# Performance work log

Hardware: AMD Instinct MI355X
Metric: run time of the kernel (lower is better)

## Reference

```python
import jax, jax.numpy as jnp
import numpy as np
from jax import lax

C = 16  # channels

def _conv1x1(x, w, b):
    # 1x1x1 Conv3d == channel-mixing einsum. x: [B,C,T,H,W], w: [O,C], b: [O]
    return jnp.einsum('oc,bcthw->bothw', w, x) + b[None, :, None, None, None]

def _ffn(x, w1, b1, w2, b2):
    return _conv1x1(jnp.tanh(_conv1x1(x, w1, b1)), w2, b2)

def setup_inputs() -> dict:
    key = jax.random.key(0)
    ks = jax.random.split(key, 12)
    s = 0.1
    x = jax.random.normal(ks[0], (2, C, 31, 256, 256), dtype=jnp.float32)
    mk_w = lambda k: jax.random.normal(k, (C, C), dtype=jnp.float32) * s
    mk_b = lambda k: jax.random.normal(k, (C,), dtype=jnp.float32) * s
    return {
        'x': x,
        'wf1': mk_w(ks[1]), 'bf1': mk_b(ks[2]),
        'wf2': mk_w(ks[3]), 'bf2': mk_b(ks[4]),
        'ww1': mk_w(ks[5]), 'bw1': mk_b(ks[6]),
        'ww2': mk_w(ks[7]), 'bw2': mk_b(ks[8]),
        'wsca': mk_w(ks[9]), 'bsca': mk_b(ks[10]),
    }

def reference(x, wf1, bf1, wf2, bf2, ww1, bw1, ww2, bw2, wsca, bsca):
    # Gates from two 1x1-conv FFNs
    Z = jnp.tanh(_ffn(x, wf1, bf1, wf2, bf2))          # [B,C,T,H,W]
    Fg = jax.nn.sigmoid(_ffn(x, ww1, bw1, ww2, bw2))   # [B,C,T,H,W]
    # Linear recurrence over time dim: h_t = f_t * h_{t-1} + (1-f_t) * z_t, h_{-1}=0
    Zt = jnp.moveaxis(Z, 2, 0)   # [T,B,C,H,W]
    Ft = jnp.moveaxis(Fg, 2, 0)
    def step(h, zf):
        z, f = zf
        h = f * h + (1.0 - f) * z
        return h, h
    h0 = jnp.zeros_like(Zt[0])
    _, hs = lax.scan(step, h0, (Zt, Ft))
    out = jnp.moveaxis(hs, 0, 2)  # [B,C,T,H,W]
    # Simplified channel attention: global avg pool -> 1x1 conv -> sigmoid -> scale
    gap = jnp.mean(out, axis=(2, 3, 4), keepdims=True)  # [B,C,1,1,1]
    att = jax.nn.sigmoid(_conv1x1(gap, wsca, bsca))
    return att * out
```

## Files before the change

### kernel.cpp

```cpp
#include <hip/hip_runtime.h>
#include <hip/hip_bf16.h>

#define TDIM 31
#define TS   65536
#define CS   (TDIM * TS)
#define BS   (16 * CS)
#define NTOT (2 * BS)
#define K1_BLOCKS 8192
#define GAP_INV (1.0f / (31.0f * 65536.0f))

typedef __attribute__((ext_vector_type(8))) short short8v;
typedef __attribute__((ext_vector_type(4))) float f32x4;
typedef __attribute__((ext_vector_type(8))) unsigned short ushort8v;

__device__ __forceinline__ float frcp(float v){ return __builtin_amdgcn_rcpf(v); }
__device__ __forceinline__ float fexp2_(float v){ return __builtin_amdgcn_exp2f(v); }
__device__ __forceinline__ float ftanh(float x){ float e = fexp2_(x*2.8853900817779268f); return 1.0f - 2.0f*frcp(e+1.0f); }
__device__ __forceinline__ float fsigm(float x){ float e = fexp2_(x*-1.4426950408889634f); return frcp(1.0f+e); }
__device__ __forceinline__ unsigned rhu16(float x){ return (__float_as_uint(x) + 0x8000u) >> 16; }
__device__ __forceinline__ float bf2f(unsigned b){ return __uint_as_float(b << 16); }

template<bool BF16H>
__global__ __launch_bounds__(256, 4) void k1_fused(
    const float* __restrict__ x,
    const float* __restrict__ wf1, const float* __restrict__ bf1,
    const float* __restrict__ wf2, const float* __restrict__ bf2,
    const float* __restrict__ ww1, const float* __restrict__ bw1,
    const float* __restrict__ ww2, const float* __restrict__ bw2,
    float* __restrict__ out, unsigned short* __restrict__ hb,
    float* __restrict__ partials)
{
    __shared__ unsigned int sGate[TDIM][16][16];
    __shared__ alignas(16) char sAfaw[4][1280];

    const int tid  = threadIdx.x;
    const int lane = tid & 63;
    const int wv   = tid >> 6;
    const int col  = lane & 15;
    const int kg   = lane >> 4;
    const int blk  = blockIdx.x;
    const int b    = blk >> 12;
    const int p0   = (blk & 4095) << 4;

    short8v A1f, A2f, A1w, A2w, Af2, Aw2;
    {
        const int c0 = (kg & 1) * 8;
#pragma unroll
        for (int i = 0; i < 8; ++i) {
            const float w1 = wf1[col*16 + c0 + i];
            unsigned u1 = __float_as_uint(w1);
            float lo1 = w1 - __uint_as_float(u1 & 0xFFFF0000u);
            A1f[i] = (short)(u1 >> 16);
            A2f[i] = (short)(__float_as_uint(lo1) >> 16);
            const float w2 = ww1[col*16 + c0 + i];
            unsigned u2 = __float_as_uint(w2);
            float lo2 = w2 - __uint_as_float(u2 & 0xFFFF0000u);
            A1w[i] = (short)(u2 >> 16);
            A2w[i] = (short)(__float_as_uint(lo2) >> 16);
            const float v2f = wf2[col*16 + c0 + i];
            const float v2w = ww2[col*16 + c0 + i];
            Af2[i] = (kg < 2)  ? (short)rhu16(v2f) : (short)0;
            Aw2[i] = (kg >= 2) ? (short)rhu16(v2w) : (short)0;
        }
    }
    float b1f[4], b1w[4], b2f[4], b2w[4];
#pragma unroll
    for (int r = 0; r < 4; ++r) {
        b1f[r] = bf1[kg*4+r]; b1w[r] = bw1[kg*4+r];
        b2f[r] = bf2[kg*4+r]; b2w[r] = bw2[kg*4+r];
    }

    const f32x4 zf4 = {0.f, 0.f, 0.f, 0.f};

    auto process = [&](int u, const float* xv) {
        short8v bx;
#pragma unroll
        for (int i = 0; i < 8; ++i) {
            const unsigned uu = __float_as_uint(xv[i]);
            const float lof = xv[i] - __uint_as_float(uu & 0xFFFF0000u);
            const unsigned lob = __float_as_uint(lof) >> 16;
            const unsigned hib = uu >> 16;
            bx[i] = (short)(kg >= 2 ? lob : hib);
        }
        f32x4 accf = zf4, accw = zf4;
        accf = __builtin_amdgcn_mfma_f32_16x16x32_bf16(A1f, bx, accf, 0, 0, 0);
        accf = __builtin_amdgcn_mfma_f32_16x16x32_bf16(A2f, bx, accf, 0, 0, 0);
        accw = __builtin_amdgcn_mfma_f32_16x16x32_bf16(A1w, bx, accw, 0, 0, 0);
        accw = __builtin_amdgcn_mfma_f32_16x16x32_bf16(A2w, bx, accw, 0, 0, 0);

        const float a0 = ftanh(accf[0]+b1f[0]), a1 = ftanh(accf[1]+b1f[1]);
        const float a2 = ftanh(accf[2]+b1f[2]), a3 = ftanh(accf[3]+b1f[3]);
        const float w0 = ftanh(accw[0]+b1w[0]), w1 = ftanh(accw[1]+b1w[1]);
        const float w2 = ftanh(accw[2]+b1w[2]), w3 = ftanh(accw[3]+b1w[3]);
        char* base = sAfaw[wv] + col * 80;
        *(uint2*)(base + kg*8)      = make_uint2((rhu16(a1)<<16)|rhu16(a0), (rhu16(a3)<<16)|rhu16(a2));
        *(uint2*)(base + 48 + kg*8) = make_uint2((rhu16(w1)<<16)|rhu16(w0), (rhu16(w3)<<16)|rhu16(w2));
        const short8v b2 = *(const short8v*)(base + ((kg & 1) * 16 + (kg >> 1) * 48));
        f32x4 acz = __builtin_amdgcn_mfma_f32_16x16x32_bf16(Af2, b2, zf4, 0, 0, 0);
        f32x4 acw = __builtin_amdgcn_mfma_f32_16x16x32_bf16(Aw2, b2, zf4, 0, 0, 0);

        uint4 pk;
        {
            unsigned w_[4];
#pragma unroll
            for (int r = 0; r < 4; ++r) {
                const float z = ftanh(acz[r] + b2f[r]);
                const float f = fsigm(acw[r] + b2w[r]);
                const int   zi = (int)__builtin_rintf(z * 32767.0f);
                const unsigned fu = (unsigned)(f * 65535.0f + 0.5f);
                w_[r] = ((unsigned)zi << 16) | (fu & 0xFFFFu);
            }
            pk = make_uint4(w_[0], w_[1], w_[2], w_[3]);
        }
        *(uint4*)&sGate[u][col][kg*4] = pk;
    };

    const unsigned xbase = (unsigned)b * BS + (unsigned)p0 + (unsigned)col
                         + (unsigned)((kg & 1) * 8) * CS;
#define LOADU(dst, u_) { const float* xp = x + (size_t)xbase + (size_t)(u_) * TS; \
    _Pragma("unroll") for (int i = 0; i < 8; ++i) (dst)[i] = xp[i * CS]; }

    float xs0[8], xs1[8], xs2[8];
    LOADU(xs0, wv)
    LOADU(xs1, wv + 4)
#pragma unroll
    for (int k = 0; k < 8; ++k) {
        const int u  = wv + 4 * k;
        const int uf = u + 8;
        if ((k % 3) == 0) {
            if (uf < TDIM) LOADU(xs2, uf)
            if (u  < TDIM) process(u, xs0);
        } else if ((k % 3) == 1) {
            if (uf < TDIM) LOADU(xs0, uf)
            if (u  < TDIM) process(u, xs1);
        } else {
            if (uf < TDIM) LOADU(xs1, uf)
            if (u  < TDIM) process(u, xs2);
        }
    }
#undef LOADU
    __syncthreads();

    {
        const int c = tid >> 4, p = tid & 15;
        const unsigned oidx = (unsigned)b * BS + (unsigned)c * CS + (unsigned)p0 + (unsigned)p;
        float h = 0.f, s = 0.f;
#pragma unroll 1
        for (int t = 0; t < TDIM; ++t) {
            const int w = (int)sGate[t][p][c];
            const float z = (float)(w >> 16) * (1.0f / 32767.0f);
            const float f = (float)(w & 0xFFFF) * (1.0f / 65535.0f);
            h = fmaf(f, h - z, z);
            s += h;
            if (BF16H) hb[oidx + (unsigned)t * TS] = (unsigned short)rhu16(h);
            else       out[oidx + (unsigned)t * TS] = h;
        }
#pragma unroll
        for (int off = 8; off; off >>= 1) s += __shfl_down(s, off, 16);
        if (p == 0) partials[blk * 16 + c] = s;
    }
}

__global__ __launch_bounds__(1024) void k2_attention(
    const float* __restrict__ partials, const float* __restrict__ wsca,
    const float* __restrict__ bsca, float* __restrict__ att)
{
    __shared__ float red[2][16][32];
    __shared__ float gap[2][16];
    const int tid = threadIdx.x;
    {
        const int b = tid >> 9, c = (tid >> 5) & 15, seg = tid & 31;
        float s = 0.f;
        const float* p = partials + (size_t)(b * 4096 + seg * 128) * 16 + c;
        for (int j = 0; j < 128; ++j) s += p[j * 16];
        red[b][c][seg] = s;
    }
    __syncthreads();
    if (tid < 32) {
        const int b = tid >> 4, c = tid & 15;
        float s = 0.f;
#pragma unroll
        for (int g = 0; g < 32; ++g) s += red[b][c][g];
        gap[b][c] = s * GAP_INV;
    }
    __syncthreads();
    if (tid < 32) {
        const int b = tid >> 4, o = tid & 15;
        float acc = bsca[o];
#pragma unroll
        for (int c = 0; c < 16; ++c) acc = fmaf(wsca[o*16 + c], gap[b][c], acc);
        att[b*16 + o] = fsigm(acc);
    }
}

__global__ __launch_bounds__(1024) void k3_scale_b(
    const unsigned short* __restrict__ hb, const float* __restrict__ att,
    float* __restrict__ out)
{
    const int bc = blockIdx.y;
    const float a = att[bc];
    const unsigned i = blockIdx.x * 1024 + threadIdx.x;
    const size_t base = (size_t)bc * CS;
    const ushort8v v = ((const ushort8v*)(hb + base))[i];
    float4 o1, o2;
    o1.x = bf2f(v[0])*a; o1.y = bf2f(v[1])*a; o1.z = bf2f(v[2])*a; o1.w = bf2f(v[3])*a;
    o2.x = bf2f(v[4])*a; o2.y = bf2f(v[5])*a; o2.z = bf2f(v[6])*a; o2.w = bf2f(v[7])*a;
    float4* op = (float4*)(out + base);
    op[i*2]     = o1;
    op[i*2 + 1] = o2;
}

__global__ __launch_bounds__(1024) void k3_scale_a(
    const float* __restrict__ att, float* __restrict__ out)
{
    const int bc = blockIdx.y;
    const float a = att[bc];
    const unsigned i = blockIdx.x * 1024 + threadIdx.x;
    float4* op = (float4*)(out + (size_t)bc * CS);
    float4 v1 = op[i*2], v2 = op[i*2 + 1];
    v1.x *= a; v1.y *= a; v1.z *= a; v1.w *= a;
    v2.x *= a; v2.y *= a; v2.z *= a; v2.w *= a;
    op[i*2] = v1; op[i*2 + 1] = v2;
}

extern "C" void kernel_launch(void* const* d_in, const int* in_sizes, int n_in,
                              void* d_out, int out_size, void* d_ws, size_t ws_size,
                              hipStream_t stream) {
    const float* x    = (const float*)d_in[0];
    const float* wf1  = (const float*)d_in[1];
    const float* bf1  = (const float*)d_in[2];
    const float* wf2  = (const float*)d_in[3];
    const float* bf2  = (const float*)d_in[4];
    const float* ww1  = (const float*)d_in[5];
    const float* bw1  = (const float*)d_in[6];
    const float* ww2  = (const float*)d_in[7];
    const float* bw2  = (const float*)d_in[8];
    const float* wsca = (const float*)d_in[9];
    const float* bsca = (const float*)d_in[10];
    float* out = (float*)d_out;

    const size_t hbBytes   = (size_t)NTOT * 2;
    const size_t partBytes = (size_t)K1_BLOCKS * 16 * 4;
    const bool bf16h = ws_size >= hbBytes + partBytes + 256;

    unsigned short* hb = (unsigned short*)d_ws;
    float* partials = bf16h ? (float*)((char*)d_ws + hbBytes) : (float*)d_ws;
    float* att = partials + K1_BLOCKS * 16;

    if (bf16h) {
        k1_fused<true><<<K1_BLOCKS, 256, 0, stream>>>(x, wf1, bf1, wf2, bf2,
            ww1, bw1, ww2, bw2, out, hb, partials);
        k2_attention<<<1, 1024, 0, stream>>>(partials, wsca, bsca, att);
        k3_scale_b<<<dim3(248, 32), 1024, 0, stream>>>(hb, att, out);
    } else {
        k1_fused<false><<<K1_BLOCKS, 256, 0, stream>>>(x, wf1, bf1, wf2, bf2,
            ww1, bw1, ww2, bw2, out, hb, partials);
        k2_attention<<<1, 1024, 0, stream>>>(partials, wsca, bsca, att);
        k3_scale_a<<<dim3(248, 32), 1024, 0, stream>>>(att, out);
    }
}
```

Before: 357.6 us.

## Deepen x prefetch, fold biases into MFMA accumulators, pack scan onto one wave

Raises the x-load prefetch depth from two to three timesteps ahead using four register buffers. It also folds the bias adds into the MFMA accumulator init, builds the bf16 hi/lo split with byte-permute instructions, and shrinks the LDS staging stride. The recurrence scan now runs on only 64 threads, each handling 4 channels with vectorized LDS reads. That cuts scan-phase threads by 4x, which risks serializing the store-heavy scan and increases register pressure.

```diff
diff --git a/kernel.cpp b/kernel.cpp
--- a/kernel.cpp
+++ b/kernel.cpp
@@ -19,6 +19,7 @@
 __device__ __forceinline__ float fsigm(float x){ float e = fexp2_(x*-1.4426950408889634f); return frcp(1.0f+e); }
 __device__ __forceinline__ unsigned rhu16(float x){ return (__float_as_uint(x) + 0x8000u) >> 16; }
 __device__ __forceinline__ float bf2f(unsigned b){ return __uint_as_float(b << 16); }
+__device__ __forceinline__ unsigned pkhi(unsigned u0, unsigned u1){ return __builtin_amdgcn_perm(u1, u0, 0x07060302u); }
 
 template<bool BF16H>
 __global__ __launch_bounds__(256, 4) void k1_fused(
@@ -31,13 +32,14 @@
     float* __restrict__ partials)
 {
     __shared__ unsigned int sGate[TDIM][16][16];
-    __shared__ alignas(16) char sAfaw[4][1280];
+    __shared__ alignas(16) char sAfaw[4][1024];
 
     const int tid  = threadIdx.x;
     const int lane = tid & 63;
     const int wv   = tid >> 6;
     const int col  = lane & 15;
     const int kg   = lane >> 4;
+    const bool lok = (kg >= 2);
     const int blk  = blockIdx.x;
     const int b    = blk >> 12;
     const int p0   = (blk & 4095) << 4;
@@ -63,56 +65,57 @@
             Aw2[i] = (kg >= 2) ? (short)rhu16(v2w) : (short)0;
         }
     }
-    float b1f[4], b1w[4], b2f[4], b2w[4];
+    f32x4 b1fv, b1wv, b2fv, b2wv;
 #pragma unroll
     for (int r = 0; r < 4; ++r) {
-        b1f[r] = bf1[kg*4+r]; b1w[r] = bw1[kg*4+r];
-        b2f[r] = bf2[kg*4+r]; b2w[r] = bw2[kg*4+r];
-    }
-
-    const f32x4 zf4 = {0.f, 0.f, 0.f, 0.f};
+        b1fv[r] = bf1[kg*4+r]; b1wv[r] = bw1[kg*4+r];
+        b2fv[r] = bf2[kg*4+r]; b2wv[r] = bw2[kg*4+r];
+    }
 
     auto process = [&](int u, const float* xv) {
-        short8v bx;
-#pragma unroll
-        for (int i = 0; i < 8; ++i) {
-            const unsigned uu = __float_as_uint(xv[i]);
-            const float lof = xv[i] - __uint_as_float(uu & 0xFFFF0000u);
-            const unsigned lob = __float_as_uint(lof) >> 16;
-            const unsigned hib = uu >> 16;
-            bx[i] = (short)(kg >= 2 ? lob : hib);
-        }
-        f32x4 accf = zf4, accw = zf4;
+        unsigned H[4], L[4];
+#pragma unroll
+        for (int j = 0; j < 4; ++j) {
+            const unsigned u0 = __float_as_uint(xv[2*j]);
+            const unsigned u1 = __float_as_uint(xv[2*j+1]);
+            const float l0 = xv[2*j]   - __uint_as_float(u0 & 0xFFFF0000u);
+            const float l1 = xv[2*j+1] - __uint_as_float(u1 & 0xFFFF0000u);
+            H[j] = pkhi(u0, u1);
+            L[j] = pkhi(__float_as_uint(l0), __float_as_uint(l1));
+        }
+        uint4 bxu;
+        bxu.x = lok ? L[0] : H[0]; bxu.y = lok ? L[1] : H[1];
+        bxu.z = lok ? L[2] : H[2]; bxu.w = lok ? L[3] : H[3];
+        const short8v bx = __builtin_bit_cast(short8v, bxu);
+
+        f32x4 accf = b1fv, accw = b1wv;
         accf = __builtin_amdgcn_mfma_f32_16x16x32_bf16(A1f, bx, accf, 0, 0, 0);
         accf = __builtin_amdgcn_mfma_f32_16x16x32_bf16(A2f, bx, accf, 0, 0, 0);
         accw = __builtin_amdgcn_mfma_f32_16x16x32_bf16(A1w, bx, accw, 0, 0, 0);
         accw = __builtin_amdgcn_mfma_f32_16x16x32_bf16(A2w, bx, accw, 0, 0, 0);
 
-        const float a0 = ftanh(accf[0]+b1f[0]), a1 = ftanh(accf[1]+b1f[1]);
-        const float a2 = ftanh(accf[2]+b1f[2]), a3 = ftanh(accf[3]+b1f[3]);
-        const float w0 = ftanh(accw[0]+b1w[0]), w1 = ftanh(accw[1]+b1w[1]);
-        const float w2 = ftanh(accw[2]+b1w[2]), w3 = ftanh(accw[3]+b1w[3]);
-        char* base = sAfaw[wv] + col * 80;
+        const float a0 = ftanh(accf[0]), a1 = ftanh(accf[1]);
+        const float a2 = ftanh(accf[2]), a3 = ftanh(accf[3]);
+        const float w0 = ftanh(accw[0]), w1 = ftanh(accw[1]);
+        const float w2 = ftanh(accw[2]), w3 = ftanh(accw[3]);
+        char* base = sAfaw[wv] + col * 64;
         *(uint2*)(base + kg*8)      = make_uint2((rhu16(a1)<<16)|rhu16(a0), (rhu16(a3)<<16)|rhu16(a2));
-        *(uint2*)(base + 48 + kg*8) = make_uint2((rhu16(w1)<<16)|rhu16(w0), (rhu16(w3)<<16)|rhu16(w2));
-        const short8v b2 = *(const short8v*)(base + ((kg & 1) * 16 + (kg >> 1) * 48));
-        f32x4 acz = __builtin_amdgcn_mfma_f32_16x16x32_bf16(Af2, b2, zf4, 0, 0, 0);
-        f32x4 acw = __builtin_amdgcn_mfma_f32_16x16x32_bf16(Aw2, b2, zf4, 0, 0, 0);
-
-        uint4 pk;
-        {
-            unsigned w_[4];
-#pragma unroll
-            for (int r = 0; r < 4; ++r) {
-                const float z = ftanh(acz[r] + b2f[r]);
-                const float f = fsigm(acw[r] + b2w[r]);
-                const int   zi = (int)__builtin_rintf(z * 32767.0f);
-                const unsigned fu = (unsigned)(f * 65535.0f + 0.5f);
-                w_[r] = ((unsigned)zi << 16) | (fu & 0xFFFFu);
-            }
-            pk = make_uint4(w_[0], w_[1], w_[2], w_[3]);
-        }
-        *(uint4*)&sGate[u][col][kg*4] = pk;
+        *(uint2*)(base + 32 + kg*8) = make_uint2((rhu16(w1)<<16)|rhu16(w0), (rhu16(w3)<<16)|rhu16(w2));
+        const short8v b2 = *(const short8v*)(base + ((kg & 1) * 16 + (kg >> 1) * 32));
+        f32x4 acz = b2fv, acw = b2wv;
+        acz = __builtin_amdgcn_mfma_f32_16x16x32_bf16(Af2, b2, acz, 0, 0, 0);
+        acw = __builtin_amdgcn_mfma_f32_16x16x32_bf16(Aw2, b2, acw, 0, 0, 0);
+
+        unsigned w_[4];
+#pragma unroll
+        for (int r = 0; r < 4; ++r) {
+            const float z = ftanh(acz[r]);
+            const float f = fsigm(acw[r]);
+            const int   zi = (int)__builtin_rintf(z * 32767.0f);
+            const unsigned fu = (unsigned)(f * 65535.0f + 0.5f);
+            w_[r] = ((unsigned)zi << 16) | (fu & 0xFFFFu);
+        }
+        *(uint4*)&sGate[u][col][kg*4] = make_uint4(w_[0], w_[1], w_[2], w_[3]);
     };
 
     const unsigned xbase = (unsigned)b * BS + (unsigned)p0 + (unsigned)col
@@ -120,44 +123,52 @@
 #define LOADU(dst, u_) { const float* xp = x + (size_t)xbase + (size_t)(u_) * TS; \
     _Pragma("unroll") for (int i = 0; i < 8; ++i) (dst)[i] = xp[i * CS]; }
 
-    float xs0[8], xs1[8], xs2[8];
+    float xs0[8], xs1[8], xs2[8], xs3[8];
     LOADU(xs0, wv)
     LOADU(xs1, wv + 4)
+    LOADU(xs2, wv + 8)
 #pragma unroll
     for (int k = 0; k < 8; ++k) {
         const int u  = wv + 4 * k;
-        const int uf = u + 8;
-        if ((k % 3) == 0) {
-            if (uf < TDIM) LOADU(xs2, uf)
-            if (u  < TDIM) process(u, xs0);
-        } else if ((k % 3) == 1) {
-            if (uf < TDIM) LOADU(xs0, uf)
-            if (u  < TDIM) process(u, xs1);
-        } else {
-            if (uf < TDIM) LOADU(xs1, uf)
-            if (u  < TDIM) process(u, xs2);
+        const int uf = u + 12;
+        switch (k & 3) {
+            case 0: if (uf < TDIM) LOADU(xs3, uf) if (u < TDIM) process(u, xs0); break;
+            case 1: if (uf < TDIM) LOADU(xs0, uf) if (u < TDIM) process(u, xs1); break;
+            case 2: if (uf < TDIM) LOADU(xs1, uf) if (u < TDIM) process(u, xs2); break;
+            default:if (uf < TDIM) LOADU(xs2, uf) if (u < TDIM) process(u, xs3); break;
         }
     }
 #undef LOADU
     __syncthreads();
 
-    {
-        const int c = tid >> 4, p = tid & 15;
-        const unsigned oidx = (unsigned)b * BS + (unsigned)c * CS + (unsigned)p0 + (unsigned)p;
-        float h = 0.f, s = 0.f;
+    if (tid < 64) {
+        const int cg = tid >> 4, p = tid & 15;
+        const unsigned obase = (unsigned)b * BS + (unsigned)p0 + (unsigned)p;
+        float h[4] = {0.f,0.f,0.f,0.f}, s[4] = {0.f,0.f,0.f,0.f};
 #pragma unroll 1
         for (int t = 0; t < TDIM; ++t) {
-            const int w = (int)sGate[t][p][c];
-            const float z = (float)(w >> 16) * (1.0f / 32767.0f);
-            const float f = (float)(w & 0xFFFF) * (1.0f / 65535.0f);
-            h = fmaf(f, h - z, z);
-            s += h;
-            if (BF16H) hb[oidx + (unsigned)t * TS] = (unsigned short)rhu16(h);
-            else       out[oidx + (unsigned)t * TS] = h;
-        }
-#pragma unroll
-        for (int off = 8; off; off >>= 1) s += __shfl_down(s, off, 16);
-        if (p == 0) partials[blk * 16 + c] = s;
+            const uint4 w4 = *(const uint4*)&sGate[t][p][cg*4];
+#pragma unroll
+            for (int j = 0; j < 4; ++j) {
+                const int w = (int)(j==0 ? w4.x : j==1 ? w4.y : j==2 ? w4.z : w4.w);
+                const float z = (float)(w >> 16) * (1.0f / 32767.0f);
+                const float f = (float)(w & 0xFFFF) * (1.0f / 65535.0f);
+                h[j] = fmaf(f, h[j] - z, z);
+                s[j] += h[j];
+                const unsigned oidx = obase + (unsigned)(cg*4+j) * CS + (unsigned)t * TS;
+                if (BF16H) hb[oidx] = (unsigned short)rhu16(h[j]);
+                else       out[oidx] = h[j];
+            }
+        }
+#pragma unroll
+        for (int j = 0; j < 4; ++j) {
+#pragma unroll
+            for (int off = 8; off; off >>= 1) s[j] += __shfl_down(s[j], off, 16);
+        }
+        if (p == 0) {
+#pragma unroll
+            for (int j = 0; j < 4; ++j) partials[blk * 16 + cg*4 + j] = s[j];
+        }
     }
 }
 
```

Result: no change. 352.4 us (-1.5%).
